# Optimization experiments

Hardware: AMD Instinct MI355X
Metric: run time of the kernel (lower is better)

Reference implementation:

```python
import jax, jax.numpy as jnp
import numpy as np

BINS = 10
MMT = 0.9
N = 33554432  # 2^25 elements


def setup_inputs() -> dict:
    key = jax.random.key(0)
    k1, k2, k3 = jax.random.split(key, 3)
    pred = jax.random.normal(k1, (N,), dtype=jnp.float32)
    target = jax.random.randint(k2, (N,), 0, 2, dtype=jnp.int32)
    acc_sum = jax.random.uniform(k3, (BINS,), dtype=jnp.float32)
    return {"pred": pred, "target": target, "acc_sum": acc_sum}


def reference(pred, target, acc_sum):
    bins = acc_sum.shape[0]
    # border = arange(bins+1)/bins, with last edge nudged up by 1e-6
    border = jnp.arange(bins + 1, dtype=jnp.float32) / bins
    border = border.at[-1].add(1e-6)

    t = target.astype(jnp.float32)
    # gradient density measure on detached predictions
    g = jnp.abs(jax.nn.sigmoid(jax.lax.stop_gradient(pred)) - t)
    # bin index: g in [border[i], border[i+1])  ->  i
    idx = jnp.clip(jnp.searchsorted(border, g, side='right') - 1, 0, bins - 1)

    # single-pass histogram (replaces the per-bin mask loop)
    counts = jax.ops.segment_sum(jnp.ones_like(g), idx, num_segments=bins)
    nonempty = counts > 0

    # momentum-accumulated bin statistics (only updated for non-empty bins)
    acc_new = jnp.where(nonempty, MMT * acc_sum + (1.0 - MMT) * counts, acc_sum)

    tot = jnp.float32(max(pred.shape[0], 1.0))
    safe_acc = jnp.where(nonempty, acc_new, 1.0)
    bin_w = jnp.where(nonempty, tot / safe_acc, 0.0)  # [bins]

    n = jnp.sum(nonempty.astype(jnp.float32))
    bin_w = jnp.where(n > 0, bin_w / jnp.maximum(n, 1.0), bin_w)

    # per-element GHM weights are constants w.r.t. pred (buffer + detached g)
    w = jax.lax.stop_gradient(bin_w[idx])

    # BCE-with-logits, numerically stable
    bce = jnp.maximum(pred, 0.0) - pred * t + jnp.log1p(jnp.exp(-jnp.abs(pred)))
    return jnp.sum(w * bce) / tot
```

## Files before the change

### kernel.cpp

```cpp
#include <hip/hip_runtime.h>

#define BINS 10
#define NTHREADS 256
#define LOG2E 1.44269504f
#define KBIAS 1024.0f
#define TILE_ELEMS (NTHREADS * 64)
#define ROUNDS 8


#define GHM_C1  2.19722458f
#define GHM_C2  1.38629436f
#define GHM_C3  0.84729786f
#define GHM_C4  0.40546511f
#define GHM_C5  0.0f
#define GHM_C6 -0.40546511f
#define GHM_C7 -0.84729786f
#define GHM_C8 -1.38629436f
#define GHM_C9 -2.19722458f

__device__ __forceinline__ float wave_reduce_add(float v) {
#pragma unroll
    for (int off = 32; off > 0; off >>= 1) v += __shfl_down(v, off, 64);
    return v;
}
__device__ __forceinline__ unsigned int wave_reduce_addu(unsigned int v) {
#pragma unroll
    for (int off = 32; off > 0; off >>= 1) v += __shfl_down((int)v, off, 64);
    return v;
}

__global__ __launch_bounds__(NTHREADS, 6) void ghm_pass1(
    const float* __restrict__ pred, const int* __restrict__ target,
    float* __restrict__ g_T,
    unsigned int* __restrict__ g_C,
    int n)
{
    float T0 = 0.f;
    float Tb[9];
#pragma unroll
    for (int b = 0; b < 9; ++b) Tb[b] = 0.f;

    const int tid    = threadIdx.x;
    const int ntiles = n / TILE_ELEMS;

#define GHM_ELEM(x_, t_)                                                     \
    {                                                                        \
        const float x = (x_);                                                \
        const float y = ((t_) != 0) ? x : -x;                                \
        const float E = __builtin_amdgcn_exp2f(y * -LOG2E);                  \
        const float r1 = 1.0f + E;                                           \
        const float bce2 = __builtin_amdgcn_logf(r1);                        \
        const float ad = bce2 + KBIAS;                                       \
        T0 += bce2;                                                          \
        Tb[0] += (y <= GHM_C1) ? ad : 0.f;                                   \
        Tb[1] += (y <= GHM_C2) ? ad : 0.f;                                   \
        Tb[2] += (y <= GHM_C3) ? ad : 0.f;                                   \
        Tb[3] += (y <= GHM_C4) ? ad : 0.f;                                   \
        Tb[4] += (y <= GHM_C5) ? ad : 0.f;                                   \
        Tb[5] += (y <= GHM_C6) ? ad : 0.f;                                   \
        Tb[6] += (y <= GHM_C7) ? ad : 0.f;                                   \
        Tb[7] += (y <= GHM_C8) ? ad : 0.f;                                   \
        Tb[8] += (y <= GHM_C9) ? ad : 0.f;                                   \
    }

#define GHM_BODY(xv, tv)                                                     \
    {                                                                        \
        GHM_ELEM((xv).x, (tv).x); GHM_ELEM((xv).y, (tv).y);                  \
        GHM_ELEM((xv).z, (tv).z); GHM_ELEM((xv).w, (tv).w);                  \
    }

    for (int tile = blockIdx.x; tile < ntiles; tile += gridDim.x) {
        const float4* __restrict__ p4 =
            reinterpret_cast<const float4*>(pred) + (size_t)tile * (TILE_ELEMS / 4) + tid * 2;
        const int4* __restrict__ t4 =
            reinterpret_cast<const int4*>(target) + (size_t)tile * (TILE_ELEMS / 4) + tid * 2;

        float4 xa0 = p4[0], xa1 = p4[1];
        int4   ta0 = t4[0], ta1 = t4[1];
        for (int r = 1; r < ROUNDS; ++r) {
            const int o = r * (NTHREADS * 2);
            const float4 xb0 = p4[o], xb1 = p4[o + 1];
            const int4   tb0 = t4[o], tb1 = t4[o + 1];
            GHM_BODY(xa0, ta0);
            GHM_BODY(xa1, ta1);
            xa0 = xb0; xa1 = xb1; ta0 = tb0; ta1 = tb1;
        }
        GHM_BODY(xa0, ta0);
        GHM_BODY(xa1, ta1);
    }

    if (blockIdx.x == gridDim.x - 1) {
        for (int i = ntiles * TILE_ELEMS + tid; i < n; i += NTHREADS) {
            GHM_ELEM(pred[i], target[i]);
        }
    }
#undef GHM_BODY
#undef GHM_ELEM

    float        sums[BINS];
    unsigned int cnts[BINS];
    sums[0] = T0; cnts[0] = 0u;
#pragma unroll
    for (int b = 1; b < BINS; ++b) {
        const float cf = floorf(Tb[b - 1] * (1.0f / KBIAS));
        cnts[b] = (unsigned int)cf;
        sums[b] = Tb[b - 1] - KBIAS * cf;
    }

    __shared__ float        r_T[BINS];
    __shared__ unsigned int r_C[BINS];
    if (tid < BINS) { r_T[tid] = 0.f; r_C[tid] = 0u; }
    __syncthreads();

    const int lane = tid & 63;
#pragma unroll
    for (int b = 0; b < BINS; ++b) {
        const float        v = wave_reduce_add(sums[b]);
        const unsigned int c = (b > 0) ? wave_reduce_addu(cnts[b]) : 0u;
        if (lane == 0) {
            atomicAdd(&r_T[b], v);
            if (b > 0) atomicAdd(&r_C[b], c);
        }
    }
    __syncthreads();

    if (tid < BINS) {
        atomicAdd(&g_T[tid], r_T[tid]);
        atomicAdd(&g_C[tid], r_C[tid]);
    }
}

__global__ void ghm_finalize(const float* __restrict__ g_T,
                             const unsigned int* __restrict__ g_C,
                             const float* __restrict__ acc_sum,
                             float* __restrict__ out, float tot, unsigned int ntot)
{
    if (threadIdx.x == 0 && blockIdx.x == 0) {
        const float LN2 = 0.69314718056f;
        float S[BINS];
        float cntf[BINS];
#pragma unroll
        for (int b = 0; b < BINS; ++b) {
            const float        Tc = g_T[b];
            const float        Tn = (b + 1 < BINS) ? g_T[b + 1] : 0.f;
            const unsigned int Cc = (b == 0) ? ntot : g_C[b];
            const unsigned int Cn = (b + 1 < BINS) ? g_C[b + 1] : 0u;
            S[b]    = (Tc - Tn) * LN2;
            cntf[b] = (float)(Cc - Cn);
        }
        float binw[BINS];
        int nne = 0;
#pragma unroll
        for (int b = 0; b < BINS; ++b) {
            const bool ne = (cntf[b] > 0.0f);
            const float accn = ne ? (0.9f * acc_sum[b] + 0.1f * cntf[b]) : acc_sum[b];
            binw[b] = ne ? (tot / accn) : 0.0f;
            nne += ne ? 1 : 0;
        }
        const float scale = (nne > 0) ? (1.0f / (float)nne) : 1.0f;
        float res = 0.0f;
#pragma unroll
        for (int b = 0; b < BINS; ++b) res += (binw[b] * scale) * S[b];
        out[0] = res / tot;
    }
}

extern "C" void kernel_launch(void* const* d_in, const int* in_sizes, int n_in,
                              void* d_out, int out_size, void* d_ws, size_t ws_size,
                              hipStream_t stream) {
    const float* pred    = (const float*)d_in[0];
    const int*   target  = (const int*)d_in[1];
    const float* acc_sum = (const float*)d_in[2];
    float*       out     = (float*)d_out;

    const int n = in_sizes[0];

    float*        g_T = (float*)d_ws;
    unsigned int* g_C = (unsigned int*)((float*)d_ws + BINS);

    hipMemsetAsync(d_ws, 0, 2 * BINS * sizeof(float), stream);

    ghm_pass1<<<2048, NTHREADS, 0, stream>>>(pred, target, g_T, g_C, n);

    const float tot = (float)(n > 1 ? n : 1);
    ghm_finalize<<<1, 64, 0, stream>>>(g_T, g_C, acc_sum, out, tot, (unsigned int)n);
}
```

Baseline: 90.20 us.

## Software-pipeline loads with inline asm, one tile per block, log2-domain thresholds

Replaces the grid-stride tile loop with one tile per block (grid = ntiles). Each thread keeps four in-flight dwordx4 load pairs issued via inline asm, with explicit vmcnt waits, to deepen memory-level parallelism. Comparisons now run in the log2-scaled domain, which saves one multiply per element. The change risks fragility: the inline asm assumes 32-bit offsets and SGPR base pointers, and ntiles=2048 blocks at 64 elems/thread matches the previous grid. Coalescing changes from 2 float4 per thread per round to 1 float4 per thread per round.

```diff
diff --git a/kernel.cpp b/kernel.cpp
--- a/kernel.cpp
+++ b/kernel.cpp
@@ -5,18 +5,11 @@
 #define LOG2E 1.44269504f
 #define KBIAS 1024.0f
 #define TILE_ELEMS (NTHREADS * 64)
-#define ROUNDS 8
+#define ROUND_BYTES (NTHREADS * 16)
 
 
-#define GHM_C1  2.19722458f
-#define GHM_C2  1.38629436f
-#define GHM_C3  0.84729786f
-#define GHM_C4  0.40546511f
-#define GHM_C5  0.0f
-#define GHM_C6 -0.40546511f
-#define GHM_C7 -0.84729786f
-#define GHM_C8 -1.38629436f
-#define GHM_C9 -2.19722458f
+typedef float        f32x4 __attribute__((ext_vector_type(4)));
+typedef unsigned int u32x4 __attribute__((ext_vector_type(4)));
 
 __device__ __forceinline__ float wave_reduce_add(float v) {
 #pragma unroll
@@ -43,58 +36,75 @@
     const int tid    = threadIdx.x;
     const int ntiles = n / TILE_ELEMS;
 
-#define GHM_ELEM(x_, t_)                                                     \
-    {                                                                        \
-        const float x = (x_);                                                \
-        const float y = ((t_) != 0) ? x : -x;                                \
-        const float E = __builtin_amdgcn_exp2f(y * -LOG2E);                  \
-        const float r1 = 1.0f + E;                                           \
-        const float bce2 = __builtin_amdgcn_logf(r1);                        \
-        const float ad = bce2 + KBIAS;                                       \
-        T0 += bce2;                                                          \
-        Tb[0] += (y <= GHM_C1) ? ad : 0.f;                                   \
-        Tb[1] += (y <= GHM_C2) ? ad : 0.f;                                   \
-        Tb[2] += (y <= GHM_C3) ? ad : 0.f;                                   \
-        Tb[3] += (y <= GHM_C4) ? ad : 0.f;                                   \
-        Tb[4] += (y <= GHM_C5) ? ad : 0.f;                                   \
-        Tb[5] += (y <= GHM_C6) ? ad : 0.f;                                   \
-        Tb[6] += (y <= GHM_C7) ? ad : 0.f;                                   \
-        Tb[7] += (y <= GHM_C8) ? ad : 0.f;                                   \
-        Tb[8] += (y <= GHM_C9) ? ad : 0.f;                                   \
+#define GHM_ELEM(x_, tu_)                                                   \
+    {                                                                       \
+        const float z = (x_) * LOG2E;                                       \
+        const float w = ((tu_) != 0u) ? z : -z;                             \
+        const float E = __builtin_amdgcn_exp2f(-w);                         \
+        const float bce2 = __builtin_amdgcn_logf(1.0f + E);                 \
+        const float ad = bce2 + KBIAS;                                      \
+        T0 += bce2;                                                         \
+        Tb[0] += (w <=  3.16992500f) ? ad : 0.f;                            \
+        Tb[1] += (w <=  2.0f)        ? ad : 0.f;                            \
+        Tb[2] += (w <=  1.22239242f) ? ad : 0.f;                            \
+        Tb[3] += (w <=  0.58496250f) ? ad : 0.f;                            \
+        Tb[4] += (w <=  0.0f)        ? ad : 0.f;                            \
+        Tb[5] += (w <= -0.58496250f) ? ad : 0.f;                            \
+        Tb[6] += (w <= -1.22239242f) ? ad : 0.f;                            \
+        Tb[7] += (w <= -2.0f)        ? ad : 0.f;                            \
+        Tb[8] += (w <= -3.16992500f) ? ad : 0.f;                            \
     }
 
-#define GHM_BODY(xv, tv)                                                     \
-    {                                                                        \
-        GHM_ELEM((xv).x, (tv).x); GHM_ELEM((xv).y, (tv).y);                  \
-        GHM_ELEM((xv).z, (tv).z); GHM_ELEM((xv).w, (tv).w);                  \
+#define COMPUTE(X, Tv)                                                      \
+    {                                                                       \
+        GHM_ELEM((X)[0], (Tv)[0]); GHM_ELEM((X)[1], (Tv)[1]);               \
+        GHM_ELEM((X)[2], (Tv)[2]); GHM_ELEM((X)[3], (Tv)[3]);               \
     }
 
-    for (int tile = blockIdx.x; tile < ntiles; tile += gridDim.x) {
-        const float4* __restrict__ p4 =
-            reinterpret_cast<const float4*>(pred) + (size_t)tile * (TILE_ELEMS / 4) + tid * 2;
-        const int4* __restrict__ t4 =
-            reinterpret_cast<const int4*>(target) + (size_t)tile * (TILE_ELEMS / 4) + tid * 2;
+#define ISSUE(X, Tv, off)                                                   \
+    asm volatile("global_load_dwordx4 %0, %2, %3\n\t"                       \
+                 "global_load_dwordx4 %1, %2, %4"                           \
+                 : "=&v"(X), "=&v"(Tv)                                      \
+                 : "v"(off), "s"(pred), "s"(target))
 
-        float4 xa0 = p4[0], xa1 = p4[1];
-        int4   ta0 = t4[0], ta1 = t4[1];
-        for (int r = 1; r < ROUNDS; ++r) {
-            const int o = r * (NTHREADS * 2);
-            const float4 xb0 = p4[o], xb1 = p4[o + 1];
-            const int4   tb0 = t4[o], tb1 = t4[o + 1];
-            GHM_BODY(xa0, ta0);
-            GHM_BODY(xa1, ta1);
-            xa0 = xb0; xa1 = xb1; ta0 = tb0; ta1 = tb1;
+#define VWAIT(nn)                                                           \
+    do { asm volatile("s_waitcnt vmcnt(" #nn ")" ::: "memory");             \
+         __builtin_amdgcn_sched_barrier(0); } while (0)
+
+    if (blockIdx.x < (unsigned)ntiles) {
+        unsigned int voff = (unsigned)blockIdx.x * (TILE_ELEMS * 4u)
+                          + (unsigned)tid * 16u;
+        f32x4 x0, x1, x2, x3;
+        u32x4 t0, t1, t2, t3;
+
+        ISSUE(x0, t0, voff); voff += ROUND_BYTES;
+        ISSUE(x1, t1, voff); voff += ROUND_BYTES;
+        ISSUE(x2, t2, voff); voff += ROUND_BYTES;
+        ISSUE(x3, t3, voff); voff += ROUND_BYTES;
+
+#pragma unroll 1
+        for (int g = 0; g < 3; ++g) {
+            VWAIT(6); COMPUTE(x0, t0); ISSUE(x0, t0, voff); voff += ROUND_BYTES;
+            VWAIT(6); COMPUTE(x1, t1); ISSUE(x1, t1, voff); voff += ROUND_BYTES;
+            VWAIT(6); COMPUTE(x2, t2); ISSUE(x2, t2, voff); voff += ROUND_BYTES;
+            VWAIT(6); COMPUTE(x3, t3); ISSUE(x3, t3, voff); voff += ROUND_BYTES;
         }
-        GHM_BODY(xa0, ta0);
-        GHM_BODY(xa1, ta1);
+        VWAIT(6); COMPUTE(x0, t0);
+        VWAIT(4); COMPUTE(x1, t1);
+        VWAIT(2); COMPUTE(x2, t2);
+        VWAIT(0); COMPUTE(x3, t3);
     }
 
     if (blockIdx.x == gridDim.x - 1) {
         for (int i = ntiles * TILE_ELEMS + tid; i < n; i += NTHREADS) {
-            GHM_ELEM(pred[i], target[i]);
+            const float xs = pred[i];
+            const unsigned int tu = (unsigned int)target[i];
+            GHM_ELEM(xs, tu);
         }
     }
-#undef GHM_BODY
+#undef ISSUE
+#undef VWAIT
+#undef COMPUTE
 #undef GHM_ELEM
 
     float        sums[BINS];
@@ -174,13 +184,15 @@
     float*       out     = (float*)d_out;
 
     const int n = in_sizes[0];
+    const int ntiles = n / TILE_ELEMS;
+    const int grid = (ntiles > 0) ? ntiles : 1;
 
     float*        g_T = (float*)d_ws;
     unsigned int* g_C = (unsigned int*)((float*)d_ws + BINS);
 
     hipMemsetAsync(d_ws, 0, 2 * BINS * sizeof(float), stream);
 
-    ghm_pass1<<<2048, NTHREADS, 0, stream>>>(pred, target, g_T, g_C, n);
+    ghm_pass1<<<grid, NTHREADS, 0, stream>>>(pred, target, g_T, g_C, n);
 
     const float tot = (float)(n > 1 ? n : 1);
     ghm_finalize<<<1, 64, 0, stream>>>(g_T, g_C, acc_sum, out, tot, (unsigned int)n);
```

After: 84.05 us (median of 2 runs). 6.8% less time.
